# Performance work log

Hardware: AMD Instinct MI355X
Metric: run time of the kernel (lower is better)

## Reference

```python
import jax, jax.numpy as jnp
import numpy as np

MAX_DISP = 4  # init kwarg maxDisplacement


def setup_inputs() -> dict:
    key = jax.random.key(0)
    k1, k2 = jax.random.split(key)
    F1 = jax.random.normal(k1, (8, 128, 128, 128), dtype=jnp.float32)
    F2 = jax.random.normal(k2, (8, 128, 128, 128), dtype=jnp.float32)
    return {"F1": F1, "F2": F2}


def reference(F1, F2):
    d = MAX_DISP
    B, H, W, C = F1.shape
    # Zero-pad F2 spatially by d on each side (NHWC)
    padded = jnp.pad(F2, ((0, 0), (d, d), (d, d), (0, 0)))
    max_offset = 2 * d + 1
    # For each (dy, dx) shift: channel-mean of F1 * shifted-F2 -> [B,H,W]
    costs = [
        jnp.mean(F1 * padded[:, y:y + H, x:x + W, :], axis=3)
        for y in range(max_offset)
        for x in range(max_offset)
    ]
    cost_volume = jnp.stack(costs, axis=3)  # [B, H, W, max_offset^2]
    return jax.nn.leaky_relu(cost_volume, negative_slope=0.1)
```

## Files before the change

### kernel.cpp

```cpp
#include <hip/hip_runtime.h>
#include <hip/hip_bf16.h>
#include <string.h>

typedef __attribute__((ext_vector_type(8))) short bf16x8;
typedef __attribute__((ext_vector_type(4))) float f32x4;

namespace {
constexpr int B = 8, H = 128, W = 128, C = 128;
constexpr int MO = 9, NOFF = 81;
constexpr int ROWS = 4;
constexpr int WCOLS = 16;
constexpr int F2R = 12;
constexpr int SREAL = 24;
constexpr int NT = 256;
constexpr int NLD = 9;
constexpr int KSTR = SREAL * 32;
constexpr int ROWSTR = 4 * KSTR;
constexpr int PADS = 256;
}

__device__ inline unsigned bf2pack(float a, float b) {
  __hip_bfloat162 h = __float22bfloat162_rn(float2{a, b});
  unsigned r;
  memcpy(&r, &h, sizeof(r));
  return r;
}

__device__ __forceinline__ f32x4 mfma16(bf16x8 a, bf16x8 b, f32x4 c) {
  return __builtin_amdgcn_mfma_f32_16x16x32_bf16(a, b, c, 0, 0, 0);
}

__global__ __launch_bounds__(NT, 2) void costvol_kernel(
    const float* __restrict__ F1, const float* __restrict__ F2,
    float* __restrict__ out)
{
  __shared__ __align__(16) short sF2[F2R * ROWSTR + PADS];

  const int lin  = blockIdx.x;
  const int b    = lin & 7;
  const int tile = lin >> 3;
  const int rt   = tile & 31;
  const int wt   = tile >> 5;
  const int h0   = rt * ROWS;
  const int wb0  = wt * WCOLS;

  const int tid  = threadIdx.x;
  const int r    = tid >> 6;
  const int lane = tid & 63;
  const int j    = lane & 15;
  const int kq   = lane >> 4;

  int gofs[NLD]; int lofs[NLD]; unsigned okm = 0;
#pragma unroll
  for (int it = 0; it < NLD; ++it) {
    const int idx  = tid + it * NT;
    const int kg   = idx & 7;
    const int slot = idx >> 3;
    const int ry   = slot / SREAL;
    const int s    = slot - ry * SREAL;
    const int fy   = h0 - 4 + ry;
    const int fx   = wb0 - 4 + s;
    const bool ok  = ((unsigned)fy < (unsigned)H) && ((unsigned)fx < (unsigned)W);
    okm |= (unsigned)ok << it;
    gofs[it] = ok ? (((b * H + fy) * W + fx) * C + kg * 4) : 0;
    lofs[it] = ry * ROWSTR + s * 32 + kg * 4;
  }

  auto issue = [&](int g, float4* ld) {
#pragma unroll
    for (int it = 0; it < NLD; ++it) {
      ld[it] = *reinterpret_cast<const float4*>(F2 + gofs[it] + g * 32);
    }
    __builtin_amdgcn_sched_barrier(0);
  };
  auto pack = [&](int g, const float4* ld) {
#pragma unroll
    for (int it = 0; it < NLD; ++it) {
      if ((okm >> it) & 1u) {
        uint2 p;
        p.x = bf2pack(ld[it].x, ld[it].y);
        p.y = bf2pack(ld[it].z, ld[it].w);
        *reinterpret_cast<uint2*>(&sF2[lofs[it] + g * KSTR]) = p;
      }
    }
  };

  float4 ldA[NLD], ldB[NLD];
  issue(0, ldA);
  issue(1, ldB);
#pragma unroll
  for (int it = 0; it < NLD; ++it) {
    if (!((okm >> it) & 1u)) {
#pragma unroll
      for (int g = 0; g < 4; ++g) {
        *reinterpret_cast<uint2*>(&sF2[lofs[it] + g * KSTR]) = uint2{0u, 0u};
      }
    }
  }
  pack(0, ldA);
  issue(2, ldA);
  pack(1, ldB);
  issue(3, ldB);
  pack(2, ldA);

  const float* f1p = F1 + (((size_t)b * H + h0 + r) * W + wb0 + j) * C + kq * 8;
  float4 u0[4], u1[4];
#pragma unroll
  for (int kk = 0; kk < 4; ++kk) {
    u0[kk] = *reinterpret_cast<const float4*>(f1p + kk * 32);
    u1[kk] = *reinterpret_cast<const float4*>(f1p + kk * 32 + 4);
  }
  __builtin_amdgcn_sched_barrier(0);
  pack(3, ldB);

  bf16x8 afrag[4];
  constexpr float S = 0.0078125f;
#pragma unroll
  for (int kk = 0; kk < 4; ++kk) {
    uint4 q;
    q.x = bf2pack(u0[kk].x * S, u0[kk].y * S);
    q.y = bf2pack(u0[kk].z * S, u0[kk].w * S);
    q.z = bf2pack(u1[kk].x * S, u1[kk].y * S);
    q.w = bf2pack(u1[kk].z * S, u1[kk].w * S);
    afrag[kk] = __builtin_bit_cast(bf16x8, q);
  }

  __syncthreads();

  f32x4 acc[9][2];
#pragma unroll
  for (int d = 0; d < 9; ++d) { acc[d][0] = {0,0,0,0}; acc[d][1] = {0,0,0,0}; }

  const short* bb = sF2 + j * 32 + kq * 8;
  __builtin_amdgcn_s_setprio(1);
#pragma unroll
  for (int kk = 0; kk < 4; ++kk) {
    const short* bk = bb + kk * KSTR;
#pragma unroll
    for (int dy = 0; dy < 9; ++dy) {
      const short* brow = bk + (r + dy) * ROWSTR;
      const bf16x8 b0 = *reinterpret_cast<const bf16x8*>(brow);
      const bf16x8 b1 = *reinterpret_cast<const bf16x8*>(brow + 512);
      acc[dy][0] = mfma16(afrag[kk], b0, acc[dy][0]);
      acc[dy][1] = mfma16(afrag[kk], b1, acc[dy][1]);
    }
  }
  __builtin_amdgcn_s_setprio(0);

  const int h = h0 + r;
  float* lb = out + (((size_t)b * H + h) * W + wb0) * NOFF + kq * 320 + j;
#pragma unroll
  for (int t = 0; t < 2; ++t) {
#pragma unroll
    for (int reg = 0; reg < 4; ++reg) {
      const int dxl = j + 16 * t - kq * 4 - reg;
      if ((unsigned)dxl <= 8u) {
#pragma unroll
        for (int dy = 0; dy < 9; ++dy) {
          float m = acc[dy][t][reg];
          m = fmaxf(m, 0.1f * m);
          lb[reg * 80 + 16 * t + dy * 9] = m;
        }
      }
    }
  }
}

extern "C" void kernel_launch(void* const* d_in, const int* in_sizes, int n_in,
                              void* d_out, int out_size, void* d_ws, size_t ws_size,
                              hipStream_t stream) {
  const float* F1 = (const float*)d_in[0];
  const float* F2 = (const float*)d_in[1];
  float* out = (float*)d_out;
  dim3 grid(B * (H / ROWS) * (W / WCOLS));
  dim3 block(NT);
  hipLaunchKernelGGL(costvol_kernel, grid, block, 0, stream, F1, F2, out);
}
```

Measured before the change: 43.27 us.

## Make blocks persistent over width tiles with double-buffered F2 staging

Each block now walks all 8 width tiles of a 4-row strip instead of handling a single tile. The next tile's F2 and F1 global loads are issued before the MFMA loop and packed into an alternate LDS buffer afterward, so load latency overlaps compute. The grid shrinks to 256 blocks, occupancy drops to one block per CU, and LDS use doubles through dynamic shared memory. The risk is underfilling the GPU with fewer blocks and higher register pressure from holding 36 float4 loads in flight.

After: 65.41 us. 1.51x slower.

```diff
diff --git a/kernel.cpp b/kernel.cpp
--- a/kernel.cpp
+++ b/kernel.cpp
@@ -7,16 +7,18 @@
 
 namespace {
 constexpr int B = 8, H = 128, W = 128, C = 128;
-constexpr int MO = 9, NOFF = 81;
+constexpr int NOFF = 81;
 constexpr int ROWS = 4;
 constexpr int WCOLS = 16;
 constexpr int F2R = 12;
 constexpr int SREAL = 24;
 constexpr int NT = 256;
 constexpr int NLD = 9;
-constexpr int KSTR = SREAL * 32;
+constexpr int KSTR = 768;
 constexpr int ROWSTR = 4 * KSTR;
-constexpr int PADS = 256;
+constexpr int BUFS = F2R * ROWSTR + 256;
+constexpr int NTILE = 8;
+constexpr int SMEM_BYTES = 2 * BUFS * 2;
 }
 
 __device__ inline unsigned bf2pack(float a, float b) {
@@ -30,19 +32,16 @@
   return __builtin_amdgcn_mfma_f32_16x16x32_bf16(a, b, c, 0, 0, 0);
 }
 
-__global__ __launch_bounds__(NT, 2) void costvol_kernel(
+__global__ __launch_bounds__(NT, 1) void costvol_kernel(
     const float* __restrict__ F1, const float* __restrict__ F2,
     float* __restrict__ out)
 {
-  __shared__ __align__(16) short sF2[F2R * ROWSTR + PADS];
+  extern __shared__ __align__(16) short sF2[];
 
-  const int lin  = blockIdx.x;
-  const int b    = lin & 7;
-  const int tile = lin >> 3;
-  const int rt   = tile & 31;
-  const int wt   = tile >> 5;
-  const int h0   = rt * ROWS;
-  const int wb0  = wt * WCOLS;
+  const int lin = blockIdx.x;
+  const int b   = lin & 7;
+  const int rt  = lin >> 3;
+  const int h0  = rt * ROWS;
 
   const int tid  = threadIdx.x;
   const int r    = tid >> 6;
@@ -50,7 +49,7 @@
   const int j    = lane & 15;
   const int kq   = lane >> 4;
 
-  int gofs[NLD]; int lofs[NLD]; unsigned okm = 0;
+  int rbase[NLD]; int lofs[NLD]; int sarr[NLD]; unsigned okyM = 0;
 #pragma unroll
   for (int it = 0; it < NLD; ++it) {
     const int idx  = tid + it * NT;
@@ -59,110 +58,125 @@
     const int ry   = slot / SREAL;
     const int s    = slot - ry * SREAL;
     const int fy   = h0 - 4 + ry;
-    const int fx   = wb0 - 4 + s;
-    const bool ok  = ((unsigned)fy < (unsigned)H) && ((unsigned)fx < (unsigned)W);
-    okm |= (unsigned)ok << it;
-    gofs[it] = ok ? (((b * H + fy) * W + fx) * C + kg * 4) : 0;
-    lofs[it] = ry * ROWSTR + s * 32 + kg * 4;
+    const bool oky = (unsigned)fy < 128u;
+    okyM |= (unsigned)oky << it;
+    sarr[it]  = s;
+    rbase[it] = ((b * H + (oky ? fy : 0)) * W + (s - 4)) * C + kg * 4;
+    lofs[it]  = ry * ROWSTR + s * 32 + kg * 4;
   }
+  auto okm_of = [&](int wt) -> unsigned {
+    unsigned m = okyM;
+    if (wt == 0) {
+#pragma unroll
+      for (int it = 0; it < NLD; ++it) if (sarr[it] < 4) m &= ~(1u << it);
+    }
+    if (wt == 7) {
+#pragma unroll
+      for (int it = 0; it < NLD; ++it) if (sarr[it] >= 20) m &= ~(1u << it);
+    }
+    return m;
+  };
 
-  auto issue = [&](int g, float4* ld) {
+  const float* f1b = F1 + (((size_t)b * H + h0 + r) * W + j) * C + kq * 8;
+  float* outb = out + (((size_t)b * H + h0 + r) * W) * NOFF + kq * 320 + j;
+
+  float4 ldv[36];
+  float4 fu0[4], fu1[4];
+  bf16x8 afrag[4];
+  unsigned okmN;
+
+  auto issue_tile = [&](int wt) {
+    okmN = okm_of(wt);
 #pragma unroll
     for (int it = 0; it < NLD; ++it) {
-      ld[it] = *reinterpret_cast<const float4*>(F2 + gofs[it] + g * 32);
+      const int go = ((okmN >> it) & 1u) ? (rbase[it] + wt * 2048) : 0;
+#pragma unroll
+      for (int g = 0; g < 4; ++g) {
+        ldv[g * 9 + it] = *reinterpret_cast<const float4*>(F2 + go + g * 32);
+      }
+    }
+    const float* f1p = f1b + wt * 2048;
+#pragma unroll
+    for (int kk = 0; kk < 4; ++kk) {
+      fu0[kk] = *reinterpret_cast<const float4*>(f1p + kk * 32);
+      fu1[kk] = *reinterpret_cast<const float4*>(f1p + kk * 32 + 4);
     }
     __builtin_amdgcn_sched_barrier(0);
   };
-  auto pack = [&](int g, const float4* ld) {
+  auto pack_tile = [&](int buf) {
+    short* dst = sF2 + buf * BUFS;
 #pragma unroll
     for (int it = 0; it < NLD; ++it) {
-      if ((okm >> it) & 1u) {
-        uint2 p;
-        p.x = bf2pack(ld[it].x, ld[it].y);
-        p.y = bf2pack(ld[it].z, ld[it].w);
-        *reinterpret_cast<uint2*>(&sF2[lofs[it] + g * KSTR]) = p;
+      const bool ok = (okmN >> it) & 1u;
+#pragma unroll
+      for (int g = 0; g < 4; ++g) {
+        uint2 p{0u, 0u};
+        if (ok) {
+          const float4 v = ldv[g * 9 + it];
+          p.x = bf2pack(v.x, v.y);
+          p.y = bf2pack(v.z, v.w);
+        }
+        *reinterpret_cast<uint2*>(dst + lofs[it] + g * KSTR) = p;
       }
+    }
+    constexpr float S = 0.0078125f;
+#pragma unroll
+    for (int kk = 0; kk < 4; ++kk) {
+      uint4 q;
+      q.x = bf2pack(fu0[kk].x * S, fu0[kk].y * S);
+      q.y = bf2pack(fu0[kk].z * S, fu0[kk].w * S);
+      q.z = bf2pack(fu1[kk].x * S, fu1[kk].y * S);
+      q.w = bf2pack(fu1[kk].z * S, fu1[kk].w * S);
+      afrag[kk] = __builtin_bit_cast(bf16x8, q);
     }
   };
 
-  float4 ldA[NLD], ldB[NLD];
-  issue(0, ldA);
-  issue(1, ldB);
+  issue_tile(0);
+  pack_tile(0);
+  __syncthreads();
+
+  for (int tt = 0; tt < NTILE; ++tt) {
+    if (tt < NTILE - 1) issue_tile(tt + 1);
+
+    f32x4 acc[9][2];
 #pragma unroll
-  for (int it = 0; it < NLD; ++it) {
-    if (!((okm >> it) & 1u)) {
+    for (int d = 0; d < 9; ++d) { acc[d][0] = {0,0,0,0}; acc[d][1] = {0,0,0,0}; }
+
+    const bf16x8 a0 = afrag[0], a1 = afrag[1], a2 = afrag[2], a3 = afrag[3];
+    const short* bb = sF2 + (tt & 1) * BUFS + j * 32 + kq * 8;
 #pragma unroll
-      for (int g = 0; g < 4; ++g) {
-        *reinterpret_cast<uint2*>(&sF2[lofs[it] + g * KSTR]) = uint2{0u, 0u};
+    for (int kk = 0; kk < 4; ++kk) {
+      const bf16x8 af = (kk == 0) ? a0 : (kk == 1) ? a1 : (kk == 2) ? a2 : a3;
+      const short* bk = bb + kk * KSTR;
+#pragma unroll
+      for (int dy = 0; dy < 9; ++dy) {
+        const short* brow = bk + (r + dy) * ROWSTR;
+        const bf16x8 b0 = *reinterpret_cast<const bf16x8*>(brow);
+        const bf16x8 b1 = *reinterpret_cast<const bf16x8*>(brow + 512);
+        acc[dy][0] = mfma16(af, b0, acc[dy][0]);
+        acc[dy][1] = mfma16(af, b1, acc[dy][1]);
       }
     }
-  }
-  pack(0, ldA);
-  issue(2, ldA);
-  pack(1, ldB);
-  issue(3, ldB);
-  pack(2, ldA);
 
-  const float* f1p = F1 + (((size_t)b * H + h0 + r) * W + wb0 + j) * C + kq * 8;
-  float4 u0[4], u1[4];
+    if (tt < NTILE - 1) pack_tile((tt + 1) & 1);
+
+    float* lb = outb + tt * (WCOLS * NOFF);
 #pragma unroll
-  for (int kk = 0; kk < 4; ++kk) {
-    u0[kk] = *reinterpret_cast<const float4*>(f1p + kk * 32);
-    u1[kk] = *reinterpret_cast<const float4*>(f1p + kk * 32 + 4);
-  }
-  __builtin_amdgcn_sched_barrier(0);
-  pack(3, ldB);
-
-  bf16x8 afrag[4];
-  constexpr float S = 0.0078125f;
+    for (int t = 0; t < 2; ++t) {
 #pragma unroll
-  for (int kk = 0; kk < 4; ++kk) {
-    uint4 q;
-    q.x = bf2pack(u0[kk].x * S, u0[kk].y * S);
-    q.y = bf2pack(u0[kk].z * S, u0[kk].w * S);
-    q.z = bf2pack(u1[kk].x * S, u1[kk].y * S);
-    q.w = bf2pack(u1[kk].z * S, u1[kk].w * S);
-    afrag[kk] = __builtin_bit_cast(bf16x8, q);
-  }
-
-  __syncthreads();
-
-  f32x4 acc[9][2];
+      for (int reg = 0; reg < 4; ++reg) {
+        const int dxl = j + 16 * t - kq * 4 - reg;
+        if ((unsigned)dxl <= 8u) {
 #pragma unroll
-  for (int d = 0; d < 9; ++d) { acc[d][0] = {0,0,0,0}; acc[d][1] = {0,0,0,0}; }
-
-  const short* bb = sF2 + j * 32 + kq * 8;
-  __builtin_amdgcn_s_setprio(1);
-#pragma unroll
-  for (int kk = 0; kk < 4; ++kk) {
-    const short* bk = bb + kk * KSTR;
-#pragma unroll
-    for (int dy = 0; dy < 9; ++dy) {
-      const short* brow = bk + (r + dy) * ROWSTR;
-      const bf16x8 b0 = *reinterpret_cast<const bf16x8*>(brow);
-      const bf16x8 b1 = *reinterpret_cast<const bf16x8*>(brow + 512);
-      acc[dy][0] = mfma16(afrag[kk], b0, acc[dy][0]);
-      acc[dy][1] = mfma16(afrag[kk], b1, acc[dy][1]);
-    }
-  }
-  __builtin_amdgcn_s_setprio(0);
-
-  const int h = h0 + r;
-  float* lb = out + (((size_t)b * H + h) * W + wb0) * NOFF + kq * 320 + j;
-#pragma unroll
-  for (int t = 0; t < 2; ++t) {
-#pragma unroll
-    for (int reg = 0; reg < 4; ++reg) {
-      const int dxl = j + 16 * t - kq * 4 - reg;
-      if ((unsigned)dxl <= 8u) {
-#pragma unroll
-        for (int dy = 0; dy < 9; ++dy) {
-          float m = acc[dy][t][reg];
-          m = fmaxf(m, 0.1f * m);
-          lb[reg * 80 + 16 * t + dy * 9] = m;
+          for (int dy = 0; dy < 9; ++dy) {
+            float m = acc[dy][t][reg];
+            m = fmaxf(m, 0.1f * m);
+            lb[reg * 80 + 16 * t + dy * 9] = m;
+          }
         }
       }
     }
+    __syncthreads();
   }
 }
 
@@ -172,7 +186,10 @@
   const float* F1 = (const float*)d_in[0];
   const float* F2 = (const float*)d_in[1];
   float* out = (float*)d_out;
-  dim3 grid(B * (H / ROWS) * (W / WCOLS));
+  hipFuncSetAttribute((const void*)costvol_kernel,
+                      hipFuncAttributeMaxDynamicSharedMemorySize, SMEM_BYTES);
+  dim3 grid(B * (H / ROWS));
   dim3 block(NT);
-  hipLaunchKernelGGL(costvol_kernel, grid, block, 0, stream, F1, F2, out);
+  hipLaunchKernelGGL(costvol_kernel, grid, block, SMEM_BYTES, stream,
+                     F1, F2, out);
 }
```

## Make blocks persistent over row strips with a ring buffer for F2 rows

Applied to the files above, without the earlier changes.

Each block now handles a 32-row strip as 8 sequential 4-row tiles instead of one tile per block. A 12-row circular shared-memory ring holds F2, so each new tile loads only 4 new rows rather than re-fetching the 8-row halo. The next tile's F2 and F1 loads are issued before the current tile's MFMA work so they overlap. This cuts halo reloads and per-block setup, but shrinks the grid from 2048 to 256 blocks, which may leave the GPU's compute units underused, and it adds extra barriers per tile.

Result: slower. 47.09 us (+8.8%).

```diff
diff --git a/kernel.cpp b/kernel.cpp
--- a/kernel.cpp
+++ b/kernel.cpp
@@ -7,16 +7,16 @@
 
 namespace {
 constexpr int B = 8, H = 128, W = 128, C = 128;
-constexpr int MO = 9, NOFF = 81;
-constexpr int ROWS = 4;
-constexpr int WCOLS = 16;
-constexpr int F2R = 12;
+constexpr int NOFF = 81;
+constexpr int NT = 256;
 constexpr int SREAL = 24;
-constexpr int NT = 256;
-constexpr int NLD = 9;
-constexpr int KSTR = SREAL * 32;
-constexpr int ROWSTR = 4 * KSTR;
+constexpr int NLD = 12;
+constexpr int KSTR = 768;
+constexpr int ROWSTR = 3072;
+constexpr int RING = 12;
 constexpr int PADS = 256;
+constexpr int RSHORTS = RING * ROWSTR + PADS;
+constexpr int NTILE = 8;
 }
 
 __device__ inline unsigned bf2pack(float a, float b) {
@@ -34,15 +34,15 @@
     const float* __restrict__ F1, const float* __restrict__ F2,
     float* __restrict__ out)
 {
-  __shared__ __align__(16) short sF2[F2R * ROWSTR + PADS];
-
-  const int lin  = blockIdx.x;
-  const int b    = lin & 7;
-  const int tile = lin >> 3;
-  const int rt   = tile & 31;
-  const int wt   = tile >> 5;
-  const int h0   = rt * ROWS;
-  const int wb0  = wt * WCOLS;
+  __shared__ __align__(16) short ring[RSHORTS];
+
+  const int lin   = blockIdx.x;
+  const int b     = lin & 7;
+  const int strip = lin >> 3;
+  const int wt    = strip & 7;
+  const int seg   = strip >> 3;
+  const int hseg  = seg * 32;
+  const int wb0   = wt * 16;
 
   const int tid  = threadIdx.x;
   const int r    = tid >> 6;
@@ -50,119 +50,141 @@
   const int j    = lane & 15;
   const int kq   = lane >> 4;
 
-  int gofs[NLD]; int lofs[NLD]; unsigned okm = 0;
-#pragma unroll
-  for (int it = 0; it < NLD; ++it) {
-    const int idx  = tid + it * NT;
-    const int kg   = idx & 7;
-    const int slot = idx >> 3;
-    const int ry   = slot / SREAL;
-    const int s    = slot - ry * SREAL;
-    const int fy   = h0 - 4 + ry;
-    const int fx   = wb0 - 4 + s;
-    const bool ok  = ((unsigned)fy < (unsigned)H) && ((unsigned)fx < (unsigned)W);
-    okm |= (unsigned)ok << it;
-    gofs[it] = ok ? (((b * H + fy) * W + fx) * C + kg * 4) : 0;
-    lofs[it] = ry * ROWSTR + s * 32 + kg * 4;
-  }
-
-  auto issue = [&](int g, float4* ld) {
+  float4 ldv[NLD];
+  unsigned okm;
+  int fybc;
+
+  auto issueF2 = [&](int fyb) {
+    fybc = fyb;
+    okm  = 0;
 #pragma unroll
     for (int it = 0; it < NLD; ++it) {
-      ld[it] = *reinterpret_cast<const float4*>(F2 + gofs[it] + g * 32);
+      const int idx = tid + it * NT;
+      const int rw  = idx / 768;
+      const int rem = idx - rw * 768;
+      const int s   = rem >> 5;
+      const int kg  = rem & 31;
+      const int fy  = fyb + rw;
+      const int fx  = wb0 - 4 + s;
+      const bool ok = ((unsigned)fy < 128u) && ((unsigned)fx < 128u);
+      okm |= (unsigned)ok << it;
+      const int ga = ((b * H + (ok ? fy : 0)) * W + (ok ? fx : 0)) * C + kg * 4;
+      ldv[it] = *reinterpret_cast<const float4*>(F2 + ga);
     }
     __builtin_amdgcn_sched_barrier(0);
   };
-  auto pack = [&](int g, const float4* ld) {
+  auto packF2 = [&]() {
 #pragma unroll
     for (int it = 0; it < NLD; ++it) {
+      const int idx  = tid + it * NT;
+      const int rw   = idx / 768;
+      const int rem  = idx - rw * 768;
+      const int s    = rem >> 5;
+      const int kg   = rem & 31;
+      const int slot = (unsigned)(fybc + rw + 48) % 12u;
+      const int lo   = slot * ROWSTR + (kg >> 3) * KSTR + s * 32 + (kg & 7) * 4;
+      uint2 p{0u, 0u};
       if ((okm >> it) & 1u) {
-        uint2 p;
-        p.x = bf2pack(ld[it].x, ld[it].y);
-        p.y = bf2pack(ld[it].z, ld[it].w);
-        *reinterpret_cast<uint2*>(&sF2[lofs[it] + g * KSTR]) = p;
+        p.x = bf2pack(ldv[it].x, ldv[it].y);
+        p.y = bf2pack(ldv[it].z, ldv[it].w);
       }
-    }
-  };
-
-  float4 ldA[NLD], ldB[NLD];
-  issue(0, ldA);
-  issue(1, ldB);
-#pragma unroll
-  for (int it = 0; it < NLD; ++it) {
-    if (!((okm >> it) & 1u)) {
-#pragma unroll
-      for (int g = 0; g < 4; ++g) {
-        *reinterpret_cast<uint2*>(&sF2[lofs[it] + g * KSTR]) = uint2{0u, 0u};
+      *reinterpret_cast<uint2*>(&ring[lo]) = p;
+    }
+  };
+
+  const float* f1b = F1 + (((size_t)b * H + hseg + r) * W + wb0 + j) * C + kq * 8;
+  float4 u0[4], u1[4];
+  auto issueF1 = [&](int tt) {
+    const float* p = f1b + (size_t)tt * 4 * W * C;
+#pragma unroll
+    for (int kk = 0; kk < 4; ++kk) {
+      u0[kk] = *reinterpret_cast<const float4*>(p + kk * 32);
+      u1[kk] = *reinterpret_cast<const float4*>(p + kk * 32 + 4);
+    }
+  };
+  bf16x8 afrag[2][4];
+  constexpr float S = 0.0078125f;
+  auto packF1 = [&](int pp) {
+#pragma unroll
+    for (int kk = 0; kk < 4; ++kk) {
+      uint4 q;
+      q.x = bf2pack(u0[kk].x * S, u0[kk].y * S);
+      q.y = bf2pack(u0[kk].z * S, u0[kk].w * S);
+      q.z = bf2pack(u1[kk].x * S, u1[kk].y * S);
+      q.w = bf2pack(u1[kk].z * S, u1[kk].w * S);
+      afrag[pp][kk] = __builtin_bit_cast(bf16x8, q);
+    }
+  };
+
+  issueF2(hseg - 4);
+  issueF1(0);
+  packF2();
+  issueF2(hseg);
+  packF1(0);
+  packF2();
+  issueF2(hseg + 4);
+  packF2();
+  __syncthreads();
+
+#pragma unroll
+  for (int tt = 0; tt < NTILE; ++tt) {
+    const int h0 = hseg + tt * 4;
+    if (tt < NTILE - 1) {
+      issueF2(h0 + 8);
+      issueF1(tt + 1);
+    }
+
+    int sofs[9];
+#pragma unroll
+    for (int dy = 0; dy < 9; ++dy) {
+      sofs[dy] = (int)((unsigned)(h0 - 4 + r + dy + 48) % 12u) * ROWSTR;
+    }
+
+    f32x4 acc[9][2];
+#pragma unroll
+    for (int d = 0; d < 9; ++d) { acc[d][0] = {0,0,0,0}; acc[d][1] = {0,0,0,0}; }
+
+    const short* bb = ring + j * 32 + kq * 8;
+    __builtin_amdgcn_s_setprio(1);
+#pragma unroll
+    for (int kk = 0; kk < 4; ++kk) {
+      const bf16x8 af = afrag[tt & 1][kk];
+      const short* bk = bb + kk * KSTR;
+#pragma unroll
+      for (int dy = 0; dy < 9; ++dy) {
+        const short* brow = bk + sofs[dy];
+        const bf16x8 b0 = *reinterpret_cast<const bf16x8*>(brow);
+        const bf16x8 b1 = *reinterpret_cast<const bf16x8*>(brow + 512);
+        acc[dy][0] = mfma16(af, b0, acc[dy][0]);
+        acc[dy][1] = mfma16(af, b1, acc[dy][1]);
       }
     }
-  }
-  pack(0, ldA);
-  issue(2, ldA);
-  pack(1, ldB);
-  issue(3, ldB);
-  pack(2, ldA);
-
-  const float* f1p = F1 + (((size_t)b * H + h0 + r) * W + wb0 + j) * C + kq * 8;
-  float4 u0[4], u1[4];
-#pragma unroll
-  for (int kk = 0; kk < 4; ++kk) {
-    u0[kk] = *reinterpret_cast<const float4*>(f1p + kk * 32);
-    u1[kk] = *reinterpret_cast<const float4*>(f1p + kk * 32 + 4);
-  }
-  __builtin_amdgcn_sched_barrier(0);
-  pack(3, ldB);
-
-  bf16x8 afrag[4];
-  constexpr float S = 0.0078125f;
-#pragma unroll
-  for (int kk = 0; kk < 4; ++kk) {
-    uint4 q;
-    q.x = bf2pack(u0[kk].x * S, u0[kk].y * S);
-    q.y = bf2pack(u0[kk].z * S, u0[kk].w * S);
-    q.z = bf2pack(u1[kk].x * S, u1[kk].y * S);
-    q.w = bf2pack(u1[kk].z * S, u1[kk].w * S);
-    afrag[kk] = __builtin_bit_cast(bf16x8, q);
-  }
-
-  __syncthreads();
-
-  f32x4 acc[9][2];
-#pragma unroll
-  for (int d = 0; d < 9; ++d) { acc[d][0] = {0,0,0,0}; acc[d][1] = {0,0,0,0}; }
-
-  const short* bb = sF2 + j * 32 + kq * 8;
-  __builtin_amdgcn_s_setprio(1);
-#pragma unroll
-  for (int kk = 0; kk < 4; ++kk) {
-    const short* bk = bb + kk * KSTR;
-#pragma unroll
-    for (int dy = 0; dy < 9; ++dy) {
-      const short* brow = bk + (r + dy) * ROWSTR;
-      const bf16x8 b0 = *reinterpret_cast<const bf16x8*>(brow);
-      const bf16x8 b1 = *reinterpret_cast<const bf16x8*>(brow + 512);
-      acc[dy][0] = mfma16(afrag[kk], b0, acc[dy][0]);
-      acc[dy][1] = mfma16(afrag[kk], b1, acc[dy][1]);
-    }
-  }
-  __builtin_amdgcn_s_setprio(0);
-
-  const int h = h0 + r;
-  float* lb = out + (((size_t)b * H + h) * W + wb0) * NOFF + kq * 320 + j;
-#pragma unroll
-  for (int t = 0; t < 2; ++t) {
-#pragma unroll
-    for (int reg = 0; reg < 4; ++reg) {
-      const int dxl = j + 16 * t - kq * 4 - reg;
-      if ((unsigned)dxl <= 8u) {
-#pragma unroll
-        for (int dy = 0; dy < 9; ++dy) {
-          float m = acc[dy][t][reg];
-          m = fmaxf(m, 0.1f * m);
-          lb[reg * 80 + 16 * t + dy * 9] = m;
+    __builtin_amdgcn_s_setprio(0);
+
+    if (tt < NTILE - 1) {
+      __syncthreads();
+      packF2();
+      packF1((tt + 1) & 1);
+    }
+
+    float* lb = out + (((size_t)b * H + h0 + r) * W + wb0) * NOFF +
+                kq * 320 + j;
+#pragma unroll
+    for (int t = 0; t < 2; ++t) {
+#pragma unroll
+      for (int reg = 0; reg < 4; ++reg) {
+        const int dxl = j + 16 * t - kq * 4 - reg;
+        if ((unsigned)dxl <= 8u) {
+#pragma unroll
+          for (int dy = 0; dy < 9; ++dy) {
+            float m = acc[dy][t][reg];
+            m = fmaxf(m, 0.1f * m);
+            lb[reg * 80 + 16 * t + dy * 9] = m;
+          }
         }
       }
     }
+    if (tt < NTILE - 1) __syncthreads();
   }
 }
 
@@ -172,7 +194,7 @@
   const float* F1 = (const float*)d_in[0];
   const float* F2 = (const float*)d_in[1];
   float* out = (float*)d_out;
-  dim3 grid(B * (H / ROWS) * (W / WCOLS));
+  dim3 grid(256);
   dim3 block(NT);
   hipLaunchKernelGGL(costvol_kernel, grid, block, 0, stream, F1, F2, out);
 }
```
